# Optimization experiments

Hardware: AMD Instinct MI355X
Metric: run time of the kernel (lower is better)

## Reference

```python
import jax, jax.numpy as jnp
import numpy as np

B, L, D, H = 4, 2048, 512, 8
DH = D // H

def cdist(x):
    # torch.cdist(x, x) with p=2: (b,l,l) euclidean distances over feature dim
    sq = jnp.sum(x * x, axis=-1)  # (b,l)
    d2 = sq[:, :, None] + sq[:, None, :] - 2.0 * jnp.einsum('bld,bmd->blm', x, x)
    return jnp.sqrt(jnp.maximum(d2, 0.0))

def distance_residual_bias(cd, mask2d):
    # raw_max=True branch
    Dm = cd * mask2d
    row_max = jnp.max(Dm, axis=-1, keepdims=True)  # (b,l,1)
    Dm = row_max - Dm
    eye = jnp.eye(Dm.shape[-1], dtype=Dm.dtype)
    Dm = Dm * (1.0 - eye)  # zero diagonal
    return Dm * mask2d

def layernorm(x, g, b, eps=1e-5):
    mu = jnp.mean(x, axis=-1, keepdims=True)
    var = jnp.mean((x - mu) ** 2, axis=-1, keepdims=True)
    return (x - mu) * jax.lax.rsqrt(var + eps) * g + b

def setup_inputs() -> dict:
    key = jax.random.key(0)
    ks = jax.random.split(key, 16)
    s = lambda k, shape: jax.random.normal(k, shape, dtype=jnp.float32) * 0.02
    inp = {
        'x': jax.random.normal(ks[0], (B, L, D), dtype=jnp.float32),
        'node_mask': jnp.ones((B, L), dtype=jnp.float32),
        'wq': s(ks[1], (D, D)), 'bq': jnp.zeros((D,), jnp.float32),
        'wk': s(ks[2], (D, D)), 'bk': jnp.zeros((D,), jnp.float32),
        'wv': s(ks[3], (D, D)), 'bv': jnp.zeros((D,), jnp.float32),
        'wo': s(ks[4], (D, D)), 'bo': jnp.zeros((D,), jnp.float32),
        'ln1_g': jnp.ones((D,), jnp.float32), 'ln1_b': jnp.zeros((D,), jnp.float32),
        'w1': s(ks[5], (D, 4 * D)), 'b1': jnp.zeros((4 * D,), jnp.float32),
        'w2': s(ks[6], (4 * D, D)), 'b2': jnp.zeros((D,), jnp.float32),
        'ln2_g': jnp.ones((D,), jnp.float32), 'ln2_b': jnp.zeros((D,), jnp.float32),
    }
    return inp

def reference(x, node_mask, wq, bq, wk, bk, wv, bv, wo, bo,
              ln1_g, ln1_b, w1, b1, w2, b2, ln2_g, ln2_b):
    b, l, d = x.shape
    mask2d = node_mask[:, :, None] * node_mask[:, None, :]  # (b,l,l)
    bias = distance_residual_bias(cdist(x), mask2d)          # (b,l,l)

    q = (x @ wq + bq).reshape(b, l, H, DH).transpose(0, 2, 1, 3)
    k = (x @ wk + bk).reshape(b, l, H, DH).transpose(0, 2, 1, 3)
    v = (x @ wv + bv).reshape(b, l, H, DH).transpose(0, 2, 1, 3)
    scores = jnp.einsum('bhqd,bhkd->bhqk', q, k) / jnp.sqrt(jnp.float32(DH))
    scores = scores + bias[:, None, :, :]  # broadcast distance bias over heads
    attn = jax.nn.softmax(scores, axis=-1)
    y = jnp.einsum('bhqk,bhkd->bhqd', attn, v).transpose(0, 2, 1, 3).reshape(b, l, d)
    y = y @ wo + bo

    X = layernorm(x + y, ln1_g, ln1_b)            # AddNorm 1 (dropout=eval/no-op)
    ffn = jax.nn.relu(X @ w1 + b1) @ w2 + b2      # PositionWiseFFN
    X = layernorm(X + ffn, ln2_g, ln2_b)          # AddNorm 2
    return X
```

## Files before the change

### kernel.cpp

```cpp
#include <hip/hip_runtime.h>
#include <stdint.h>

#define GAS __attribute__((address_space(1)))
#define LAS __attribute__((address_space(3)))

typedef __attribute__((ext_vector_type(8))) __bf16 bf16x8;
typedef __attribute__((ext_vector_type(4))) float f32x4;

static constexpr int Bb = 4, Ll = 2048, Dd = 512, Hh = 8, DHd = 64;
static constexpr float LOG2E = 1.4426950408889634f;

__device__ __forceinline__ unsigned short f2bf(float f){
  unsigned u = __float_as_uint(f);
  u += 0x7fffu + ((u >> 16) & 1u);
  return (unsigned short)(u >> 16);
}
__device__ __forceinline__ void gload16(const void* g, void* l){
  __builtin_amdgcn_global_load_lds((const GAS void*)g, (LAS void*)l, 16, 0, 0);
}
__device__ __forceinline__ f32x4 mfma16(bf16x8 a, bf16x8 b, f32x4 c){
  return __builtin_amdgcn_mfma_f32_16x16x32_bf16(a, b, c, 0, 0, 0);
}
__device__ __forceinline__ float exp2_hw(float x){
  float r; asm("v_exp_f32 %0, %1" : "=v"(r) : "v"(x)); return r;
}

__global__ __launch_bounds__(256) void sumsq_cast(const float* __restrict__ x,
                                                  unsigned short* __restrict__ xbf,
                                                  float* __restrict__ sq){
  int row = blockIdx.x, tid = threadIdx.x;
  float2 v = ((const float2*)(x + (size_t)row * Dd))[tid];
  ((unsigned*)(xbf + (size_t)row * Dd))[tid] =
      (unsigned)f2bf(v.x) | ((unsigned)f2bf(v.y) << 16);
  float s2 = v.x * v.x + v.y * v.y;
  #pragma unroll
  for (int t = 1; t < 64; t <<= 1) s2 += __shfl_xor(s2, t, 64);
  __shared__ float red[4];
  if ((tid & 63) == 0) red[tid >> 6] = s2;
  __syncthreads();
  if (tid == 0) sq[row] = red[0] + red[1] + red[2] + red[3];
}

__global__ void transpose_all(
    const float* __restrict__ wq, const float* __restrict__ wk,
    const float* __restrict__ wv, const float* __restrict__ wo,
    const float* __restrict__ w1, const float* __restrict__ w2,
    unsigned short* __restrict__ wqkvT, unsigned short* __restrict__ woT,
    unsigned short* __restrict__ w1T, unsigned short* __restrict__ w2T)
{
  __shared__ float t[32][33];
  int bid = blockIdx.x;
  const float* in; unsigned short* out; int R, C, bx, by;
  if (bid < 1024){
    int s = bid >> 8, tt = bid & 255;
    in  = s == 0 ? wq : s == 1 ? wk : s == 2 ? wv : wo;
    out = s == 3 ? woT : wqkvT + s * 512 * 512;
    R = 512; C = 512; bx = tt & 15; by = tt >> 4;
  } else if (bid < 2048){
    int tt = bid - 1024; in = w1; out = w1T; R = 512; C = 2048; bx = tt & 63; by = tt >> 6;
  } else {
    int tt = bid - 2048; in = w2; out = w2T; R = 2048; C = 512; bx = tt & 15; by = tt >> 4;
  }
  int tx = threadIdx.x, ty = threadIdx.y;
  int c0 = bx * 32, r0 = by * 32;
  #pragma unroll
  for (int j = 0; j < 32; j += 8) t[ty + j][tx] = in[(size_t)(r0 + ty + j) * C + c0 + tx];
  __syncthreads();
  #pragma unroll
  for (int j = 0; j < 32; j += 8) out[(size_t)(c0 + ty + j) * R + r0 + tx] = f2bf(t[tx][ty + j]);
}

template<int MODE>
__global__ __launch_bounds__(256) void gemm_bt(
    const unsigned short* __restrict__ A,
    const unsigned short* __restrict__ Bt,
    int M, int N, int K,
    const float* __restrict__ bias,
    const float* __restrict__ extra,
    float* __restrict__ outf,
    unsigned short* __restrict__ outb,
    const float* __restrict__ sq,
    float* __restrict__ rmax,
    const float* __restrict__ mask,
    const float* __restrict__ bias_k,
    const float* __restrict__ bias_v)
{
  int m0, n0, bxx = 0, byy = 0;
  if (MODE == 0){
    int z = blockIdx.z;
    A    += (size_t)z * Ll * Dd;
    Bt    = A;
    outb += (size_t)z * Ll * Ll;
    sq += z * Ll; rmax += z * Ll; mask += z * Ll;
    int tt = blockIdx.x, byv = 0;
    while (tt >= 16 - byv){ tt -= 16 - byv; byv++; }
    byy = byv; bxx = byv + tt;
    m0 = byy * 128; n0 = bxx * 128;
  } else {
    m0 = blockIdx.y * 128; n0 = blockIdx.x * 128;
  }
  const int tid = threadIdx.x, w = tid >> 6, l = tid & 63;
  const int wm = w >> 1, wn = w & 1;
  __shared__ unsigned short lA[2][128 * 64];
  __shared__ unsigned short lB[2][128 * 64];
  f32x4 acc[4][4];
  const f32x4 z4 = {0.f, 0.f, 0.f, 0.f};
  #pragma unroll
  for (int i = 0; i < 4; i++){
    #pragma unroll
    for (int j = 0; j < 4; j++) acc[i][j] = z4;
  }
  const int srow = w * 8 + (l >> 3);
  const int sc = l & 7;

  #pragma unroll
  for (int j = 0; j < 4; j++){
    int row = j * 32 + srow;
    gload16(A + (size_t)(m0 + row) * K + ((sc ^ (row & 7)) << 3),
            &lA[0][0] + j * 2048 + w * 512);
    gload16(Bt + (size_t)(n0 + row) * K + ((sc ^ (row & 7)) << 3),
            &lB[0][0] + j * 2048 + w * 512);
  }
  __syncthreads();

  int cur = 0;
  for (int k0 = 0; k0 < K; k0 += 64, cur ^= 1){
    if (k0 + 64 < K){
      #pragma unroll
      for (int j = 0; j < 4; j++){
        int row = j * 32 + srow;
        gload16(A + (size_t)(m0 + row) * K + k0 + 64 + ((sc ^ (row & 7)) << 3),
                &lA[cur ^ 1][0] + j * 2048 + w * 512);
        gload16(Bt + (size_t)(n0 + row) * K + k0 + 64 + ((sc ^ (row & 7)) << 3),
                &lB[cur ^ 1][0] + j * 2048 + w * 512);
      }
    }
    bf16x8 af[4][2], bv[4][2];
    #pragma unroll
    for (int kk = 0; kk < 2; kk++){
      #pragma unroll
      for (int f = 0; f < 4; f++){
        int ra = wm * 64 + f * 16 + (l & 15);
        af[f][kk] = *(const bf16x8*)((const char*)&lA[cur][0] + ra * 128 +
                      (((kk * 4 + (l >> 4)) ^ (ra & 7)) << 4));
        int rb = wn * 64 + f * 16 + (l & 15);
        bv[f][kk] = *(const bf16x8*)((const char*)&lB[cur][0] + rb * 128 +
                      (((kk * 4 + (l >> 4)) ^ (rb & 7)) << 4));
      }
    }
    #pragma unroll
    for (int mf = 0; mf < 4; mf++){
      #pragma unroll
      for (int nf = 0; nf < 4; nf++){
        #pragma unroll
        for (int kk = 0; kk < 2; kk++)
          acc[mf][nf] = mfma16(af[mf][kk], bv[nf][kk], acc[mf][nf]);
      }
    }
    __syncthreads();
  }

  if (MODE == 0){
    float sqc[4], mkc[4];
    #pragma unroll
    for (int nf = 0; nf < 4; nf++){
      int col = n0 + wn * 64 + nf * 16 + (l & 15);
      sqc[nf] = sq[col]; mkc[nf] = mask[col];
    }
    #pragma unroll
    for (int mf = 0; mf < 4; mf++){
      #pragma unroll
      for (int r = 0; r < 4; r++){
        int row = m0 + wm * 64 + mf * 16 + (l >> 4) * 4 + r;
        float sqi = sq[row], mi = mask[row];
        #pragma unroll
        for (int nf = 0; nf < 4; nf++){
          float d2 = sqi + sqc[nf] - 2.f * acc[mf][nf][r];
          acc[mf][nf][r] = sqrtf(fmaxf(d2, 0.f)) * (mi * mkc[nf]) * LOG2E + 8.f;
        }
      }
    }
    #pragma unroll
    for (int mf = 0; mf < 4; mf++){
      #pragma unroll
      for (int r = 0; r < 4; r++){
        int row = m0 + wm * 64 + mf * 16 + (l >> 4) * 4 + r;
        float rm = 0.f;
        #pragma unroll
        for (int nf = 0; nf < 4; nf++){
          int col = n0 + wn * 64 + nf * 16 + (l & 15);
          outb[(size_t)row * Ll + col] = f2bf(acc[mf][nf][r]);
          rm = fmaxf(rm, acc[mf][nf][r]);
        }
        #pragma unroll
        for (int t = 1; t < 16; t <<= 1) rm = fmaxf(rm, __shfl_xor(rm, t, 64));
        if ((l & 15) == 0) atomicMax((int*)(rmax + row), __float_as_int(rm));
      }
    }
    if (bxx != byy){
      #pragma unroll
      for (int nf = 0; nf < 4; nf++){
        int col = n0 + wn * 64 + nf * 16 + (l & 15);
        float cm = 0.f;
        #pragma unroll
        for (int mf = 0; mf < 4; mf++){
          uint2 pk2;
          pk2.x = (unsigned)f2bf(acc[mf][nf][0]) | ((unsigned)f2bf(acc[mf][nf][1]) << 16);
          pk2.y = (unsigned)f2bf(acc[mf][nf][2]) | ((unsigned)f2bf(acc[mf][nf][3]) << 16);
          int rowb = m0 + wm * 64 + mf * 16 + (l >> 4) * 4;
          *(uint2*)(outb + (size_t)col * Ll + rowb) = pk2;
          cm = fmaxf(cm, fmaxf(fmaxf(acc[mf][nf][0], acc[mf][nf][1]),
                               fmaxf(acc[mf][nf][2], acc[mf][nf][3])));
        }
        cm = fmaxf(cm, __shfl_xor(cm, 16, 64));
        cm = fmaxf(cm, __shfl_xor(cm, 32, 64));
        if ((l >> 4) == 0) atomicMax((int*)(rmax + col), __float_as_int(cm));
      }
    }
  } else {
    #pragma unroll
    for (int mf = 0; mf < 4; mf++){
      #pragma unroll
      for (int r = 0; r < 4; r++){
        int row = m0 + wm * 64 + mf * 16 + (l >> 4) * 4 + r;
        #pragma unroll
        for (int nf = 0; nf < 4; nf++){
          int col = n0 + wn * 64 + nf * 16 + (l & 15);
          float bval;
          if (MODE == 5){
            const float* bp = col < 512 ? bias : (col < 1024 ? bias_k : bias_v);
            bval = bp[col & 511];
          } else {
            bval = bias[col];
          }
          float v = acc[mf][nf][r] + bval;
          if (MODE == 3) outb[(size_t)row * N + col] = f2bf(fmaxf(v, 0.f));
          if (MODE == 5){
            if (col < 1024){
              outb[(size_t)row * N + col] = f2bf(v);
            } else {
              int c = col - 1024;
              int bidx = row >> 11, lpos = row & 2047;
              ((unsigned short*)outf)[(((size_t)bidx * Hh + (c >> 6)) * DHd + (c & 63)) * Ll + lpos] = f2bf(v);
            }
          }
          if (MODE == 2 || MODE == 4)
            outf[(size_t)row * N + col] = v + extra[(size_t)row * N + col];
        }
      }
    }
  }
}

__global__ __launch_bounds__(256) void flash_attn(
    const unsigned short* __restrict__ qkv,
    const unsigned short* __restrict__ vT,
    const unsigned short* __restrict__ cdm,
    const float* __restrict__ rmax,
    unsigned short* __restrict__ y)
{
  const int b = blockIdx.z, h = blockIdx.y, q0 = blockIdx.x * 128;
  const int tid = threadIdx.x, w = tid >> 6, l = tid & 63;
  const int ql = l & 15, lg = l >> 4;
  __shared__ unsigned short QPs[128 * 64];
  __shared__ unsigned short Ks[2][64 * 64];
  __shared__ unsigned short Vs[2][64 * 64];

  const int srow = w * 8 + (l >> 3);
  const int sc = l & 7;
  const unsigned short* kbase = qkv + (size_t)b * Ll * 1536 + 512 + h * DHd;
  const unsigned short* vbase = vT + (size_t)(b * Hh + h) * DHd * Ll;

  #pragma unroll
  for (int j = 0; j < 4; j++){
    int row = j * 32 + srow;
    gload16(qkv + (size_t)(b * Ll + q0 + row) * 1536 + h * DHd + ((sc ^ (row & 7)) << 3),
            QPs + j * 2048 + w * 512);
  }
  #pragma unroll
  for (int j = 0; j < 2; j++){
    int row = j * 32 + srow;
    gload16(kbase + (size_t)row * 1536 + ((sc ^ (row & 7)) << 3),
            &Ks[0][0] + j * 2048 + w * 512);
    gload16(vbase + (size_t)row * Ll + ((sc ^ (row & 7)) << 3),
            &Vs[0][0] + j * 2048 + w * 512);
  }

  float rmx[2]; const unsigned short* cdrow[2];
  #pragma unroll
  for (int s = 0; s < 2; s++){
    int qg = q0 + w * 32 + s * 16 + ql;
    rmx[s] = rmax[b * Ll + qg];
    cdrow[s] = cdm + (size_t)(b * Ll + qg) * Ll;
  }
  uint2 cdn[2][4];
  #pragma unroll
  for (int s = 0; s < 2; s++)
    #pragma unroll
    for (int nf = 0; nf < 4; nf++)
      cdn[s][nf] = *(const uint2*)(cdrow[s] + nf * 16 + lg * 4);

  f32x4 o[2][4];
  const f32x4 z4 = {0.f, 0.f, 0.f, 0.f};
  #pragma unroll
  for (int s = 0; s < 2; s++)
    #pragma unroll
    for (int nf = 0; nf < 4; nf++) o[s][nf] = z4;
  float lsum[2] = {0.f, 0.f};

  __syncthreads();

  bf16x8 qa[2][2];
  #pragma unroll
  for (int s = 0; s < 2; s++)
    #pragma unroll
    for (int kk = 0; kk < 2; kk++){
      int ra = w * 32 + s * 16 + ql;
      qa[s][kk] = *(const bf16x8*)((const char*)QPs + ra * 128 +
                   (((kk * 4 + lg) ^ (ra & 7)) << 4));
    }

  const int NT = Ll / 64;
  for (int t = 0; t < NT; ++t){
    const int k0 = t * 64;
    const int cur = t & 1;

    if (t + 1 < NT){
      const int kn = k0 + 64;
      #pragma unroll
      for (int j = 0; j < 2; j++){
        int row = j * 32 + srow;
        gload16(kbase + (size_t)(kn + row) * 1536 + ((sc ^ (row & 7)) << 3),
                &Ks[cur ^ 1][0] + j * 2048 + w * 512);
        gload16(vbase + (size_t)row * Ll + kn + ((sc ^ (row & 7)) << 3),
                &Vs[cur ^ 1][0] + j * 2048 + w * 512);
      }
    }

    f32x4 sa[2][4];
    #pragma unroll
    for (int s = 0; s < 2; s++)
      #pragma unroll
      for (int nf = 0; nf < 4; nf++) sa[s][nf] = z4;
    #pragma unroll
    for (int nf = 0; nf < 4; nf++){
      #pragma unroll
      for (int kk = 0; kk < 2; kk++){
        int rb = nf * 16 + ql;
        bf16x8 kb = *(const bf16x8*)((const char*)Ks[cur] + rb * 128 +
                      (((kk * 4 + lg) ^ (rb & 7)) << 4));
        sa[0][nf] = mfma16(kb, qa[0][kk], sa[0][nf]);
        sa[1][nf] = mfma16(kb, qa[1][kk], sa[1][nf]);
      }
    }

    #pragma unroll
    for (int s = 0; s < 2; s++){
      float sv[16];
      #pragma unroll
      for (int nf = 0; nf < 4; nf++){
        float c0 = __uint_as_float(cdn[s][nf].x << 16);
        float c1 = __uint_as_float(cdn[s][nf].x & 0xffff0000u);
        float c2 = __uint_as_float(cdn[s][nf].y << 16);
        float c3 = __uint_as_float(cdn[s][nf].y & 0xffff0000u);
        sv[nf * 4 + 0] = fmaf(sa[s][nf][0], 0.125f * LOG2E, -c0);
        sv[nf * 4 + 1] = fmaf(sa[s][nf][1], 0.125f * LOG2E, -c1);
        sv[nf * 4 + 2] = fmaf(sa[s][nf][2], 0.125f * LOG2E, -c2);
        sv[nf * 4 + 3] = fmaf(sa[s][nf][3], 0.125f * LOG2E, -c3);
      }
      if (t + 1 < NT){
        #pragma unroll
        for (int nf = 0; nf < 4; nf++)
          cdn[s][nf] = *(const uint2*)(cdrow[s] + k0 + 64 + nf * 16 + lg * 4);
      }
      const int dk0 = q0 + ((2 * w + s) >> 2) * 64;
      if (k0 == dk0){
        const int dn = (2 * w + s) & 3;
        #pragma unroll
        for (int r = 0; r < 4; r++)
          if (lg * 4 + r == ql) sv[dn * 4 + r] -= rmx[s];
      }
      float p[16], ps = 0.f;
      #pragma unroll
      for (int i = 0; i < 16; i++){ p[i] = exp2_hw(sv[i]); ps += p[i]; }
      lsum[s] += ps;

      const int rp = s * 16 + ql;
      #pragma unroll
      for (int nf = 0; nf < 4; nf++){
        unsigned d0, d1;
        asm("v_cvt_pk_bf16_f32 %0, %1, %2" : "=v"(d0) : "v"(p[nf*4+0]), "v"(p[nf*4+1]));
        asm("v_cvt_pk_bf16_f32 %0, %1, %2" : "=v"(d1) : "v"(p[nf*4+2]), "v"(p[nf*4+3]));
        uint2 pk2; pk2.x = d0; pk2.y = d1;
        *(uint2*)((char*)QPs + w * 4096 + rp * 128 +
                  ((nf * 32 + lg * 8) ^ ((rp & 7) << 4))) = pk2;
      }
    }

    bf16x8 pa[2][2];
    #pragma unroll
    for (int s = 0; s < 2; s++)
      #pragma unroll
      for (int kk = 0; kk < 2; kk++){
        int rp = s * 16 + ql;
        pa[s][kk] = *(const bf16x8*)((const char*)QPs + w * 4096 + rp * 128 +
                     (((kk * 4 + lg) ^ (rp & 7)) << 4));
      }
    #pragma unroll
    for (int nf = 0; nf < 4; nf++){
      #pragma unroll
      for (int kk = 0; kk < 2; kk++){
        int rv = nf * 16 + ql;
        bf16x8 vb = *(const bf16x8*)((const char*)Vs[cur] + rv * 128 +
                      (((kk * 4 + lg) ^ (rv & 7)) << 4));
        o[0][nf] = mfma16(pa[0][kk], vb, o[0][nf]);
        o[1][nf] = mfma16(pa[1][kk], vb, o[1][nf]);
      }
    }
    __syncthreads();
  }

  #pragma unroll
  for (int s = 0; s < 2; s++){
    float ltot = lsum[s];
    ltot += __shfl_xor(ltot, 16, 64);
    ltot += __shfl_xor(ltot, 32, 64);
    float lf[4];
    #pragma unroll
    for (int r = 0; r < 4; r++)
      lf[r] = __shfl(ltot, (l & 48) | (lg * 4 + r), 64);
    #pragma unroll
    for (int nf = 0; nf < 4; nf++){
      #pragma unroll
      for (int r = 0; r < 4; r++){
        int qo = q0 + w * 32 + s * 16 + lg * 4 + r;
        float v = o[s][nf][r] / lf[r];
        y[(size_t)(b * Ll + qo) * Dd + h * DHd + nf * 16 + ql] = f2bf(v);
      }
    }
  }
}

__global__ __launch_bounds__(256) void ln_kernel(const float* __restrict__ in,
                                                 const float* __restrict__ g,
                                                 const float* __restrict__ bt,
                                                 float* __restrict__ outf,
                                                 unsigned short* __restrict__ outb){
  int row = blockIdx.x, tid = threadIdx.x;
  float2 v = ((const float2*)(in + (size_t)row * Dd))[tid];
  float s = v.x + v.y, s2 = v.x * v.x + v.y * v.y;
  #pragma unroll
  for (int t = 1; t < 64; t <<= 1){ s += __shfl_xor(s, t, 64); s2 += __shfl_xor(s2, t, 64); }
  __shared__ float red[8];
  if ((tid & 63) == 0){ red[tid >> 6] = s; red[4 + (tid >> 6)] = s2; }
  __syncthreads();
  float S  = red[0] + red[1] + red[2] + red[3];
  float S2 = red[4] + red[5] + red[6] + red[7];
  float mu = S * (1.f / 512.f);
  float var = fmaxf(S2 * (1.f / 512.f) - mu * mu, 0.f);
  float rs = rsqrtf(var + 1e-5f);
  int c = tid * 2;
  float o0 = (v.x - mu) * rs * g[c] + bt[c];
  float o1 = (v.y - mu) * rs * g[c + 1] + bt[c + 1];
  float2 ov; ov.x = o0; ov.y = o1;
  ((float2*)(outf + (size_t)row * Dd))[tid] = ov;
  if (outb){
    ((unsigned*)(outb + (size_t)row * Dd))[tid] =
        (unsigned)f2bf(o0) | ((unsigned)f2bf(o1) << 16);
  }
}

extern "C" void kernel_launch(void* const* d_in, const int* in_sizes, int n_in,
                              void* d_out, int out_size, void* d_ws, size_t ws_size,
                              hipStream_t stream){
  const float* x     = (const float*)d_in[0];
  const float* nmask = (const float*)d_in[1];
  const float* wq = (const float*)d_in[2];  const float* bq = (const float*)d_in[3];
  const float* wk = (const float*)d_in[4];  const float* bk = (const float*)d_in[5];
  const float* wv = (const float*)d_in[6];  const float* bv = (const float*)d_in[7];
  const float* wo = (const float*)d_in[8];  const float* bo = (const float*)d_in[9];
  const float* ln1g = (const float*)d_in[10]; const float* ln1b = (const float*)d_in[11];
  const float* w1 = (const float*)d_in[12]; const float* b1 = (const float*)d_in[13];
  const float* w2 = (const float*)d_in[14]; const float* b2 = (const float*)d_in[15];
  const float* ln2g = (const float*)d_in[16]; const float* ln2b = (const float*)d_in[17];
  float* outp = (float*)d_out;
  char* ws = (char*)d_ws;

  unsigned short* xbf   = (unsigned short*)(ws + 0);
  float* sq   = (float*)(ws + 8388608);
  float* rmax = (float*)(ws + 8421376);
  unsigned short* wqkvT = (unsigned short*)(ws + 8454144);
  unsigned short* woT   = (unsigned short*)(ws + 10027008);
  unsigned short* w1T   = (unsigned short*)(ws + 10551296);
  unsigned short* w2T   = (unsigned short*)(ws + 12648448);
  unsigned short* cdm   = (unsigned short*)(ws + 14745600);
  unsigned short* qkv   = (unsigned short*)(ws + 48300032);
  unsigned short* vT    = (unsigned short*)(ws + 73465856);
  unsigned short* yb    = (unsigned short*)(ws + 81854464);
  float* res = (float*)(ws + 90243072);
  float* Xf  = (float*)(ws + 107020288);
  unsigned short* h1  = cdm;
  unsigned short* Xbf = qkv;

  hipMemsetAsync(rmax, 0, sizeof(float) * Bb * Ll, stream);

  sumsq_cast<<<Bb * Ll, 256, 0, stream>>>(x, xbf, sq);

  transpose_all<<<3072, dim3(32, 8), 0, stream>>>(wq, wk, wv, wo, w1, w2,
                                                  wqkvT, woT, w1T, w2T);

  gemm_bt<0><<<dim3(136, 1, 4), 256, 0, stream>>>(xbf, xbf, Ll, Ll, Dd,
      nullptr, nullptr, nullptr, cdm, sq, rmax, nmask, nullptr, nullptr);

  gemm_bt<5><<<dim3(12, 64, 1), 256, 0, stream>>>(xbf, wqkvT, Bb * Ll, 1536, Dd,
      bq, nullptr, (float*)vT, qkv, nullptr, nullptr, nullptr, bk, bv);

  flash_attn<<<dim3(Ll / 128, Hh, Bb), 256, 0, stream>>>(qkv, vT, cdm, rmax, yb);

  gemm_bt<2><<<dim3(4, 64, 1), 256, 0, stream>>>(yb, woT, Bb * Ll, Dd, Dd,
      bo, x, res, nullptr, nullptr, nullptr, nullptr, nullptr, nullptr);

  ln_kernel<<<Bb * Ll, 256, 0, stream>>>(res, ln1g, ln1b, Xf, Xbf);

  gemm_bt<3><<<dim3(16, 64, 1), 256, 0, stream>>>(Xbf, w1T, Bb * Ll, 4 * Dd, Dd,
      b1, nullptr, nullptr, h1, nullptr, nullptr, nullptr, nullptr, nullptr);
  gemm_bt<4><<<dim3(4, 64, 1), 256, 0, stream>>>(h1, w2T, Bb * Ll, Dd, 4 * Dd,
      b2, Xf, res, nullptr, nullptr, nullptr, nullptr, nullptr, nullptr);

  ln_kernel<<<Bb * Ll, 256, 0, stream>>>(res, ln2g, ln2b, outp, nullptr);
}
```

Before: 268.9 us.

## Split attention over key halves with combine kernel and separate V transpose

Flash attention now processes each key half in a separate block, doubling the grid, and writes unnormalized fp32 partial outputs and row sums, which a new combine kernel sums and normalizes into bf16. The V transpose moves from scattered stores in the QKV gemm epilogue into a dedicated LDS-based transpose kernel. V is single-buffered in LDS with an extra barrier, and occupancy is hinted at 4 blocks per CU. This aims for better CU utilization and coalesced writes, at the cost of extra fp32 partial traffic and two extra launches.

Measured after the change: 293.3 us. +9.1%, slower.

```diff
diff --git a/kernel.cpp b/kernel.cpp
--- a/kernel.cpp
+++ b/kernel.cpp
@@ -68,6 +68,42 @@
   __syncthreads();
   #pragma unroll
   for (int j = 0; j < 32; j += 8) out[(size_t)(c0 + ty + j) * R + r0 + tx] = f2bf(t[tx][ty + j]);
+}
+
+__global__ __launch_bounds__(256) void v_transpose(const unsigned short* __restrict__ qkv,
+                                                   unsigned short* __restrict__ vT){
+  int b = blockIdx.z, h = blockIdx.y, l0 = blockIdx.x * 64;
+  int tid = threadIdx.x;
+  __shared__ unsigned short t[64 * 64];
+  #pragma unroll
+  for (int it = 0; it < 2; ++it){
+    int row = tid >> 2;
+    int c = (tid & 3) + it * 4;
+    uint4 d = *(const uint4*)(qkv + (size_t)(b * Ll + l0 + row) * 1536 + 1024 + h * DHd + c * 8);
+    *(uint4*)((char*)t + row * 128 + ((c ^ (row & 7)) << 4)) = d;
+  }
+  __syncthreads();
+  #pragma unroll
+  for (int it = 0; it < 2; ++it){
+    int dh = tid >> 2;
+    int c2 = (tid & 3) + it * 4;
+    unsigned pk[4];
+    #pragma unroll
+    for (int p = 0; p < 4; ++p){
+      unsigned short e0, e1;
+      {
+        int ll = c2 * 8 + p * 2;
+        e0 = *(const unsigned short*)((const char*)t + ll * 128 +
+              ((((dh >> 3) ^ (ll & 7))) << 4) + ((dh & 7) << 1));
+        ll = c2 * 8 + p * 2 + 1;
+        e1 = *(const unsigned short*)((const char*)t + ll * 128 +
+              ((((dh >> 3) ^ (ll & 7))) << 4) + ((dh & 7) << 1));
+      }
+      pk[p] = (unsigned)e0 | ((unsigned)e1 << 16);
+    }
+    uint4 o; o.x = pk[0]; o.y = pk[1]; o.z = pk[2]; o.w = pk[3];
+    *(uint4*)(vT + ((size_t)(b * Hh + h) * DHd + dh) * Ll + l0 + c2 * 8) = o;
+  }
 }
 
 template<int MODE>
@@ -235,15 +271,7 @@
           }
           float v = acc[mf][nf][r] + bval;
           if (MODE == 3) outb[(size_t)row * N + col] = f2bf(fmaxf(v, 0.f));
-          if (MODE == 5){
-            if (col < 1024){
-              outb[(size_t)row * N + col] = f2bf(v);
-            } else {
-              int c = col - 1024;
-              int bidx = row >> 11, lpos = row & 2047;
-              ((unsigned short*)outf)[(((size_t)bidx * Hh + (c >> 6)) * DHd + (c & 63)) * Ll + lpos] = f2bf(v);
-            }
-          }
+          if (MODE == 5) outb[(size_t)row * N + col] = f2bf(v);
           if (MODE == 2 || MODE == 4)
             outf[(size_t)row * N + col] = v + extra[(size_t)row * N + col];
         }
@@ -252,24 +280,27 @@
   }
 }
 
-__global__ __launch_bounds__(256) void flash_attn(
+__global__ __launch_bounds__(256, 4) void flash_attn(
     const unsigned short* __restrict__ qkv,
     const unsigned short* __restrict__ vT,
     const unsigned short* __restrict__ cdm,
     const float* __restrict__ rmax,
-    unsigned short* __restrict__ y)
+    float* __restrict__ Opart,
+    float* __restrict__ lpart)
 {
-  const int b = blockIdx.z, h = blockIdx.y, q0 = blockIdx.x * 128;
+  const int b = blockIdx.z >> 1, half = blockIdx.z & 1;
+  const int koff = half << 10;
+  const int h = blockIdx.y, q0 = blockIdx.x * 128;
   const int tid = threadIdx.x, w = tid >> 6, l = tid & 63;
   const int ql = l & 15, lg = l >> 4;
   __shared__ unsigned short QPs[128 * 64];
   __shared__ unsigned short Ks[2][64 * 64];
-  __shared__ unsigned short Vs[2][64 * 64];
+  __shared__ unsigned short Vs[64 * 64];
 
   const int srow = w * 8 + (l >> 3);
   const int sc = l & 7;
-  const unsigned short* kbase = qkv + (size_t)b * Ll * 1536 + 512 + h * DHd;
-  const unsigned short* vbase = vT + (size_t)(b * Hh + h) * DHd * Ll;
+  const unsigned short* kbase = qkv + ((size_t)(b * Ll + koff)) * 1536 + 512 + h * DHd;
+  const unsigned short* vbase = vT + (size_t)(b * Hh + h) * DHd * Ll + koff;
 
   #pragma unroll
   for (int j = 0; j < 4; j++){
@@ -283,7 +314,7 @@
     gload16(kbase + (size_t)row * 1536 + ((sc ^ (row & 7)) << 3),
             &Ks[0][0] + j * 2048 + w * 512);
     gload16(vbase + (size_t)row * Ll + ((sc ^ (row & 7)) << 3),
-            &Vs[0][0] + j * 2048 + w * 512);
+            &Vs[0] + j * 2048 + w * 512);
   }
 
   float rmx[2]; const unsigned short* cdrow[2];
@@ -291,7 +322,7 @@
   for (int s = 0; s < 2; s++){
     int qg = q0 + w * 32 + s * 16 + ql;
     rmx[s] = rmax[b * Ll + qg];
-    cdrow[s] = cdm + (size_t)(b * Ll + qg) * Ll;
+    cdrow[s] = cdm + (size_t)(b * Ll + qg) * Ll + koff;
   }
   uint2 cdn[2][4];
   #pragma unroll
@@ -320,20 +351,17 @@
                    (((kk * 4 + lg) ^ (ra & 7)) << 4));
     }
 
-  const int NT = Ll / 64;
+  const int NT = 1024 / 64;
   for (int t = 0; t < NT; ++t){
-    const int k0 = t * 64;
+    const int k0l = t * 64;
     const int cur = t & 1;
 
     if (t + 1 < NT){
-      const int kn = k0 + 64;
       #pragma unroll
       for (int j = 0; j < 2; j++){
         int row = j * 32 + srow;
-        gload16(kbase + (size_t)(kn + row) * 1536 + ((sc ^ (row & 7)) << 3),
+        gload16(kbase + (size_t)(k0l + 64 + row) * 1536 + ((sc ^ (row & 7)) << 3),
                 &Ks[cur ^ 1][0] + j * 2048 + w * 512);
-        gload16(vbase + (size_t)row * Ll + kn + ((sc ^ (row & 7)) << 3),
-                &Vs[cur ^ 1][0] + j * 2048 + w * 512);
       }
     }
 
@@ -371,10 +399,10 @@
       if (t + 1 < NT){
         #pragma unroll
         for (int nf = 0; nf < 4; nf++)
-          cdn[s][nf] = *(const uint2*)(cdrow[s] + k0 + 64 + nf * 16 + lg * 4);
+          cdn[s][nf] = *(const uint2*)(cdrow[s] + k0l + 64 + nf * 16 + lg * 4);
       }
       const int dk0 = q0 + ((2 * w + s) >> 2) * 64;
-      if (k0 == dk0){
+      if (koff + k0l == dk0){
         const int dn = (2 * w + s) & 3;
         #pragma unroll
         for (int r = 0; r < 4; r++)
@@ -397,6 +425,8 @@
       }
     }
 
+    __syncthreads();
+
     bf16x8 pa[2][2];
     #pragma unroll
     for (int s = 0; s < 2; s++)
@@ -411,13 +441,23 @@
       #pragma unroll
       for (int kk = 0; kk < 2; kk++){
         int rv = nf * 16 + ql;
-        bf16x8 vb = *(const bf16x8*)((const char*)Vs[cur] + rv * 128 +
+        bf16x8 vb = *(const bf16x8*)((const char*)Vs + rv * 128 +
                       (((kk * 4 + lg) ^ (rv & 7)) << 4));
         o[0][nf] = mfma16(pa[0][kk], vb, o[0][nf]);
         o[1][nf] = mfma16(pa[1][kk], vb, o[1][nf]);
       }
     }
+
     __syncthreads();
+
+    if (t + 1 < NT){
+      #pragma unroll
+      for (int j = 0; j < 2; j++){
+        int row = j * 32 + srow;
+        gload16(vbase + (size_t)row * Ll + k0l + 64 + ((sc ^ (row & 7)) << 3),
+                &Vs[0] + j * 2048 + w * 512);
+      }
+    }
   }
 
   #pragma unroll
@@ -425,20 +465,38 @@
     float ltot = lsum[s];
     ltot += __shfl_xor(ltot, 16, 64);
     ltot += __shfl_xor(ltot, 32, 64);
-    float lf[4];
-    #pragma unroll
-    for (int r = 0; r < 4; r++)
-      lf[r] = __shfl(ltot, (l & 48) | (lg * 4 + r), 64);
+    if (lg == 0){
+      int qg = q0 + w * 32 + s * 16 + ql;
+      lpart[((size_t)(half * Bb + b) * Hh + h) * Ll + qg] = ltot;
+    }
     #pragma unroll
     for (int nf = 0; nf < 4; nf++){
       #pragma unroll
       for (int r = 0; r < 4; r++){
         int qo = q0 + w * 32 + s * 16 + lg * 4 + r;
-        float v = o[s][nf][r] / lf[r];
-        y[(size_t)(b * Ll + qo) * Dd + h * DHd + nf * 16 + ql] = f2bf(v);
-      }
-    }
-  }
+        Opart[((size_t)(half * Bb + b) * Ll + qo) * Dd + h * DHd + nf * 16 + ql]
+            = o[s][nf][r];
+      }
+    }
+  }
+}
+
+__global__ __launch_bounds__(256) void combine_o(
+    const float* __restrict__ Opart, const float* __restrict__ lpart,
+    unsigned short* __restrict__ y)
+{
+  int row = blockIdx.x;
+  int b = row >> 11, lq = row & 2047;
+  int tid = threadIdx.x;
+  int h = (tid * 2) >> 6;
+  float2 o0 = ((const float2*)(Opart + (size_t)row * Dd))[tid];
+  float2 o1 = ((const float2*)(Opart + ((size_t)(Bb * Ll) + row) * Dd))[tid];
+  float ls = lpart[((size_t)b * Hh + h) * Ll + lq]
+           + lpart[((size_t)(Bb + b) * Hh + h) * Ll + lq];
+  float rinv = 1.f / ls;
+  ((unsigned*)(y + (size_t)row * Dd))[tid] =
+      (unsigned)f2bf((o0.x + o1.x) * rinv) |
+      ((unsigned)f2bf((o0.y + o1.y) * rinv) << 16);
 }
 
 __global__ __launch_bounds__(256) void ln_kernel(const float* __restrict__ in,
@@ -501,6 +559,8 @@
   float* Xf  = (float*)(ws + 107020288);
   unsigned short* h1  = cdm;
   unsigned short* Xbf = qkv;
+  float* Opart = res;
+  float* lpart = (float*)xbf;
 
   hipMemsetAsync(rmax, 0, sizeof(float) * Bb * Ll, stream);
 
@@ -513,9 +573,14 @@
       nullptr, nullptr, nullptr, cdm, sq, rmax, nmask, nullptr, nullptr);
 
   gemm_bt<5><<<dim3(12, 64, 1), 256, 0, stream>>>(xbf, wqkvT, Bb * Ll, 1536, Dd,
-      bq, nullptr, (float*)vT, qkv, nullptr, nullptr, nullptr, bk, bv);
-
-  flash_attn<<<dim3(Ll / 128, Hh, Bb), 256, 0, stream>>>(qkv, vT, cdm, rmax, yb);
+      bq, nullptr, nullptr, qkv, nullptr, nullptr, nullptr, bk, bv);
+
+  v_transpose<<<dim3(Ll / 64, Hh, Bb), 256, 0, stream>>>(qkv, vT);
+
+  flash_attn<<<dim3(Ll / 128, Hh, Bb * 2), 256, 0, stream>>>(qkv, vT, cdm, rmax,
+                                                             Opart, lpart);
+
+  combine_o<<<Bb * Ll, 256, 0, stream>>>(Opart, lpart, yb);
 
   gemm_bt<2><<<dim3(4, 64, 1), 256, 0, stream>>>(yb, woT, Bb * Ll, Dd, Dd,
       bo, x, res, nullptr, nullptr, nullptr, nullptr, nullptr, nullptr);
```
